# Kernel optimization log

Measured on AMD Instinct MI355X. Metric: run time of the kernel, lower is better.

Reference implementation:

```python
import jax, jax.numpy as jnp
import numpy as np

EPS = 1e-08
K = 3  # kernel size


def _conv_same_per_sample(xi, wi):
    # xi: [Cin,H,W], wi: [Cout,Cin,K,K] -> [Cout,H,W]
    out = jax.lax.conv_general_dilated(
        xi[None],  # [1,Cin,H,W]
        wi,
        window_strides=(1, 1),
        padding=((K // 2, K // 2), (K // 2, K // 2)),
        dimension_numbers=("NCHW", "OIHW", "NCHW"),
    )
    return out[0]


def setup_inputs() -> dict:
    key = jax.random.key(0)
    ks = jax.random.split(key, 6)
    B, Cin, Cout, S, H, W = 16, 256, 256, 512, 64, 64
    x = jax.random.normal(ks[0], (B, Cin, H, W), dtype=jnp.float32)
    y = jax.random.normal(ks[1], (B, S), dtype=jnp.float32)
    weights = jax.random.normal(ks[2], (Cout, Cin, K, K), dtype=jnp.float32)
    bias = jnp.zeros((Cout,), dtype=jnp.float32)
    # nn.Linear(style_channels, in_channels)
    lim = 1.0 / np.sqrt(S)
    style_w = jax.random.uniform(ks[3], (Cin, S), jnp.float32, -lim, lim)
    style_b = jax.random.uniform(ks[4], (Cin,), jnp.float32, -lim, lim)
    return {"x": x, "y": y, "weights": weights, "bias": bias,
            "style_w": style_w, "style_b": style_b}


def reference(x, y, weights, bias, style_w, style_b):
    # style: [B, Cin]
    style = y @ style_w.T + style_b
    # modulate: [B, Cout, Cin, K, K]
    w_mod = weights[None] * style[:, None, :, None, None]
    # demodulate over (Cin, K, K)
    w_std = jnp.sqrt(jnp.sum(w_mod * w_mod, axis=(2, 3, 4), keepdims=True) + EPS)
    w_demod = w_mod / w_std
    # per-sample conv (equivalent to groups=batch grouped conv)
    out = jax.vmap(_conv_same_per_sample)(x, w_demod)  # [B,Cout,H,W]
    return out + bias[None, :, None, None]
```

## Files before the change

### kernel.cpp

```cpp
#include <hip/hip_runtime.h>

typedef __bf16 bf16;
typedef __bf16 bf16x8 __attribute__((ext_vector_type(8)));
typedef float f32x4 __attribute__((ext_vector_type(4)));

#define EPS 1e-8f

constexpr int B = 16, CI = 256, CO = 256, S = 512, H = 64, W = 64;
constexpr int PH = 66;
constexpr int TAPS = 9;

constexpr size_t WS_WD    = 0;
constexpr size_t WS_XPAD  = 1179648;
constexpr size_t WS_STYLE = WS_XPAD + (size_t)B*PH*32*PH*16;
constexpr size_t WS_WSQT  = WS_STYLE + 16384;
constexpr size_t WS_INV   = WS_WSQT + 262144;

__global__ void prep1_kernel(const float* __restrict__ y,
                             const float* __restrict__ sw,
                             const float* __restrict__ sb,
                             const float* __restrict__ wts,
                             bf16x8* __restrict__ wd,
                             float* __restrict__ wsqT,
                             float* __restrict__ style) {
    __shared__ float t[8 * 289];
    int i = blockIdx.x;
    if (i < 256) {
        int cb = i & 31;
        int ib = i >> 5;
        const float* src = wts + ((size_t)cb * 8) * (CI * TAPS) + ib * 32 * TAPS;
        for (int e = threadIdx.x; e < 8 * 288; e += 256) {
            int col = e / 288, idx = e - col * 288;
            t[col * 289 + idx] = src[(size_t)col * (CI * TAPS) + idx];
        }
        __syncthreads();
        for (int c = threadIdx.x; c < 288; c += 256) {
            int co_l = c & 7, ci8_l = (c >> 3) & 3, tap = c >> 5;
            bf16x8 v;
#pragma unroll
            for (int j = 0; j < 8; ++j) v[j] = (bf16)t[co_l * 289 + (ci8_l * 8 + j) * 9 + tap];
            wd[((size_t)tap * 32 + ib * 4 + ci8_l) * CO + cb * 8 + co_l] = v;
        }
        int c = threadIdx.x;
        int co_l = c & 7, ci_l = c >> 3;
        float s = 0.f;
#pragma unroll
        for (int tap = 0; tap < 9; ++tap) {
            float w = t[co_l * 289 + ci_l * 9 + tap];
            s += w * w;
        }
        wsqT[((size_t)(ib * 32 + ci_l)) * CO + cb * 8 + co_l] = s;
    } else {
        int i2 = i - 256;
        int b = i2 >> 6;
        int c = (i2 & 63) * 4 + (threadIdx.x >> 6);
        int lane = threadIdx.x & 63;
        const float* yr = y + (size_t)b * S;
        const float* wr = sw + (size_t)c * S;
        float acc = 0.f;
#pragma unroll
        for (int k = 0; k < 8; ++k) acc += yr[lane + k * 64] * wr[lane + k * 64];
        for (int off = 32; off; off >>= 1) acc += __shfl_down(acc, off, 64);
        if (lane == 0) style[b * CI + c] = acc + sb[c];
    }
}

__global__ void prep2_kernel(const float* __restrict__ x,
                             const float* __restrict__ style,
                             const float* __restrict__ wsqT,
                             bf16x8* __restrict__ xp,
                             float* __restrict__ invstd) {
    __shared__ float t[4][32][W + 1];
    int i = blockIdx.x;
    if (i >= 2176) {
        int b = i - 2176, co = threadIdx.x;
        const float* st = style + b * CI;
        float acc = 0.f;
        for (int ci = 0; ci < CI; ++ci) {
            float s = st[ci];
            acc += wsqT[(size_t)ci * CO + co] * s * s;
        }
        invstd[b * CO + co] = rsqrtf(acc + EPS);
        return;
    }
    int cc = i & 7;
    int u = i >> 3;
    int yb = u % 17, b = u / 17;
    bf16x8 z;
#pragma unroll
    for (int j = 0; j < 8; ++j) z[j] = (bf16)0.f;

    if (yb == 16) {
        for (int q = threadIdx.x; q < 2 * 4 * PH; q += 256) {
            int row = (q >= 4 * PH) ? (PH - 1) : 0;
            int rest = (q >= 4 * PH) ? q - 4 * PH : q;
            int sub = rest / PH, col = rest - sub * PH;
            xp[(((size_t)b * PH + row) * 32 + cc * 4 + sub) * PH + col] = z;
        }
        return;
    }

    int h0 = yb * 4;
    const float* xb = x + ((size_t)b * CI + cc * 32) * (H * W);
    const float* st = style + b * CI + cc * 32;
#pragma unroll
    for (int k = 0; k < 8; ++k) {
        int idx = threadIdx.x + k * 256;
        int w4 = idx & 15, ci = (idx >> 4) & 31, r = idx >> 9;
        f32x4 v = *(const f32x4*)(xb + ((size_t)ci * H + h0 + r) * W + w4 * 4);
        float s = st[ci];
        t[r][ci][w4 * 4 + 0] = v.x * s;
        t[r][ci][w4 * 4 + 1] = v.y * s;
        t[r][ci][w4 * 4 + 2] = v.z * s;
        t[r][ci][w4 * 4 + 3] = v.w * s;
    }
    __syncthreads();
#pragma unroll
    for (int k = 0; k < 4; ++k) {
        int q = threadIdx.x + k * 256;
        int w = q & 63, sub = (q >> 6) & 3, r = q >> 8;
        bf16x8 v;
#pragma unroll
        for (int j = 0; j < 8; ++j) v[j] = (bf16)t[r][sub * 8 + j][w];
        xp[(((size_t)b * PH + h0 + r + 1) * 32 + cc * 4 + sub) * PH + (w + 1)] = v;
    }
    if (threadIdx.x < 32) {
        int r = threadIdx.x >> 3, sub = (threadIdx.x >> 1) & 3;
        int col = (threadIdx.x & 1) ? (PH - 1) : 0;
        xp[(((size_t)b * PH + h0 + r + 1) * 32 + cc * 4 + sub) * PH + col] = z;
    }
}

__global__ void conv_kernel(const bf16x8* __restrict__ wd,
                            const bf16x8* __restrict__ xp,
                            const float* __restrict__ bias,
                            const float* __restrict__ invstd,
                            float* __restrict__ out) {
    int i = blockIdx.x;
    int xcd = i & 7, t = i >> 3;
    int b = xcd * 2 + (t >> 6);
    int rest = t & 63;
    int cotile = rest & 1, rowpair = rest >> 1;
    int tid = threadIdx.x;
    int wave = tid >> 6, lane = tid & 63;
    int co_half = wave & 1, sp_half = wave >> 1;
    int r = rowpair * 2 + sp_half;
    int co_base = cotile * 128 + co_half * 64;
    int lm = lane & 15, lk = lane >> 4;

    f32x4 acc[4][4] = {};

    const bf16x8* xpb = xp + (size_t)b * PH * 32 * PH;

#pragma unroll 1
    for (int c8 = 0; c8 < 32; c8 += 4) {
        const bf16x8* wq = wd + (size_t)(c8 + lk) * CO + co_base + lm;
        const bf16x8* xq = xpb + ((size_t)r * 32 + c8 + lk) * PH + lm;
#pragma unroll
        for (int kh = 0; kh < 3; ++kh) {
#pragma unroll
            for (int kw = 0; kw < 3; ++kw) {
                const int tap = kh * 3 + kw;
                bf16x8 av[4], bv[4];
#pragma unroll
                for (int a = 0; a < 4; ++a)
                    av[a] = wq[(size_t)tap * 32 * CO + a * 16];
#pragma unroll
                for (int j = 0; j < 4; ++j)
                    bv[j] = xq[(size_t)kh * 32 * PH + kw + j * 16];
#pragma unroll
                for (int a = 0; a < 4; ++a)
#pragma unroll
                    for (int j = 0; j < 4; ++j)
                        acc[a][j] = __builtin_amdgcn_mfma_f32_16x16x32_bf16(av[a], bv[j], acc[a][j], 0, 0, 0);
            }
        }
    }

#pragma unroll
    for (int a = 0; a < 4; ++a) {
#pragma unroll
        for (int g = 0; g < 4; ++g) {
            int co = co_base + a * 16 + lk * 4 + g;
            float sc = invstd[b * CO + co];
            float bvl = bias[co];
            size_t o = (((size_t)b * CO + co) * H + r) * W;
#pragma unroll
            for (int j = 0; j < 4; ++j)
                out[o + j * 16 + lm] = acc[a][j][g] * sc + bvl;
        }
    }
}

extern "C" void kernel_launch(void* const* d_in, const int* in_sizes, int n_in,
                              void* d_out, int out_size, void* d_ws, size_t ws_size,
                              hipStream_t stream) {
    const float* x    = (const float*)d_in[0];
    const float* y    = (const float*)d_in[1];
    const float* wts  = (const float*)d_in[2];
    const float* bias = (const float*)d_in[3];
    const float* sw   = (const float*)d_in[4];
    const float* sb   = (const float*)d_in[5];
    float* out = (float*)d_out;

    char* ws = (char*)d_ws;
    bf16x8* wd    = (bf16x8*)(ws + WS_WD);
    bf16x8* xpad  = (bf16x8*)(ws + WS_XPAD);
    float* style  = (float*)(ws + WS_STYLE);
    float* wsqT   = (float*)(ws + WS_WSQT);
    float* invstd = (float*)(ws + WS_INV);

    prep1_kernel<<<dim3(1280), dim3(256), 0, stream>>>(y, sw, sb, wts, wd, wsqT, style);
    prep2_kernel<<<dim3(2192), dim3(256), 0, stream>>>(x, style, wsqT, xpad, invstd);
    conv_kernel<<<dim3(1024), dim3(256), 0, stream>>>(wd, xpad, bias, invstd, out);
}
```

Baseline: 212.4 us.

## Double-buffer conv operand loads across taps with sched barriers

The conv inner loop is restructured into a software pipeline. Each tap's weight and input fragments are loaded into alternating register buffers one step ahead of the MFMA block that consumes the previous buffer, with sched_barrier forcing the loads to issue before the MFMAs. It also adds launch_bounds(256,2) to cap register use at two blocks per SIMD group. The aim is to hide global-load latency behind MFMA work, at the cost of extra registers and a redundant prefetch on the last iteration.

```diff
diff --git a/kernel.cpp b/kernel.cpp
--- a/kernel.cpp
+++ b/kernel.cpp
@@ -131,7 +131,22 @@
     }
 }
 
-__global__ void conv_kernel(const bf16x8* __restrict__ wd,
+#define LOAD_TAP(c8_, kh_, kw_, av_, bv_)                                         \
+    {                                                                             \
+        const bf16x8* wq_ = wbase + ((size_t)((kh_)*3 + (kw_)) * 32 + (c8_)) * CO;\
+        const bf16x8* xq_ = xbase + ((size_t)(kh_) * 32 + (c8_)) * PH + (kw_);    \
+        _Pragma("unroll") for (int a_ = 0; a_ < 4; ++a_) (av_)[a_] = wq_[a_ * 16];\
+        _Pragma("unroll") for (int j_ = 0; j_ < 4; ++j_) (bv_)[j_] = xq_[j_ * 16];\
+    }
+
+#define MFMA_STEP(av_, bv_)                                                       \
+    _Pragma("unroll") for (int a_ = 0; a_ < 4; ++a_)                              \
+        _Pragma("unroll") for (int j_ = 0; j_ < 4; ++j_)                          \
+            acc[a_][j_] = __builtin_amdgcn_mfma_f32_16x16x32_bf16(                \
+                (av_)[a_], (bv_)[j_], acc[a_][j_], 0, 0, 0);
+
+__global__ __launch_bounds__(256, 2) void conv_kernel(
+                            const bf16x8* __restrict__ wd,
                             const bf16x8* __restrict__ xp,
                             const float* __restrict__ bias,
                             const float* __restrict__ invstd,
@@ -151,28 +166,29 @@
     f32x4 acc[4][4] = {};
 
     const bf16x8* xpb = xp + (size_t)b * PH * 32 * PH;
+    const bf16x8* wbase = wd + (size_t)lk * CO + co_base + lm;
+    const bf16x8* xbase = xpb + ((size_t)r * 32 + lk) * PH + lm;
+
+    bf16x8 av0[4], bv0[4], av1[4], bv1[4];
+
+    LOAD_TAP(0, 0, 0, av0, bv0);
 
 #pragma unroll 1
-    for (int c8 = 0; c8 < 32; c8 += 4) {
-        const bf16x8* wq = wd + (size_t)(c8 + lk) * CO + co_base + lm;
-        const bf16x8* xq = xpb + ((size_t)r * 32 + c8 + lk) * PH + lm;
-#pragma unroll
-        for (int kh = 0; kh < 3; ++kh) {
-#pragma unroll
-            for (int kw = 0; kw < 3; ++kw) {
-                const int tap = kh * 3 + kw;
-                bf16x8 av[4], bv[4];
-#pragma unroll
-                for (int a = 0; a < 4; ++a)
-                    av[a] = wq[(size_t)tap * 32 * CO + a * 16];
-#pragma unroll
-                for (int j = 0; j < 4; ++j)
-                    bv[j] = xq[(size_t)kh * 32 * PH + kw + j * 16];
-#pragma unroll
-                for (int a = 0; a < 4; ++a)
-#pragma unroll
-                    for (int j = 0; j < 4; ++j)
-                        acc[a][j] = __builtin_amdgcn_mfma_f32_16x16x32_bf16(av[a], bv[j], acc[a][j], 0, 0, 0);
+    for (int c8a = 0; c8a < 32; c8a += 8) {
+#pragma unroll
+        for (int v = 0; v < 18; ++v) {
+            const int ntap = (v + 1) % 9;
+            const int nkh = ntap / 3, nkw = ntap % 3;
+            int nc8 = (v == 17) ? ((c8a + 8) & 31)
+                                : (c8a + ((v + 1) / 9) * 4);
+            if ((v & 1) == 0) {
+                LOAD_TAP(nc8, nkh, nkw, av1, bv1);
+                __builtin_amdgcn_sched_barrier(0);
+                MFMA_STEP(av0, bv0);
+            } else {
+                LOAD_TAP(nc8, nkh, nkw, av0, bv0);
+                __builtin_amdgcn_sched_barrier(0);
+                MFMA_STEP(av1, bv1);
             }
         }
     }
```

Result: faster. 201.6 us (-5.1%).
